# Optimization experiments

Hardware: AMD Instinct MI355X
Metric: run time of the kernel (lower is better)

The kernel has to match this reference:

```python
import jax, jax.numpy as jnp
import numpy as np

VOCAB, EMB, HID = 256, 32, 128
B, T = 512, 512


def setup_inputs() -> dict:
    key = jax.random.key(0)
    ks = jax.random.split(key, 8)
    s_emb = 1.0  # torch nn.Embedding default N(0,1)
    s_lstm = 1.0 / np.sqrt(HID)  # torch LSTM uniform(-1/sqrt(H), 1/sqrt(H))
    s_cls = 1.0 / np.sqrt(HID)
    return {
        "inputs": jax.random.randint(ks[0], (B, T), 0, VOCAB, dtype=jnp.int64),
        "emb": jax.random.normal(ks[1], (VOCAB, EMB), jnp.float32) * s_emb,
        "W_ih": jax.random.uniform(ks[2], (4 * HID, EMB), jnp.float32, -s_lstm, s_lstm),
        "W_hh": jax.random.uniform(ks[3], (4 * HID, HID), jnp.float32, -s_lstm, s_lstm),
        "b_ih": jax.random.uniform(ks[4], (4 * HID,), jnp.float32, -s_lstm, s_lstm),
        "b_hh": jax.random.uniform(ks[5], (4 * HID,), jnp.float32, -s_lstm, s_lstm),
        "W_cls": jax.random.uniform(ks[6], (VOCAB, HID), jnp.float32, -s_cls, s_cls),
        "b_cls": jax.random.uniform(ks[7], (VOCAB,), jnp.float32, -s_cls, s_cls),
    }


def reference(inputs, emb, W_ih, W_hh, b_ih, b_hh, W_cls, b_cls):
    x = emb[inputs]  # [B, T, E]
    H = W_hh.shape[1]
    # Precompute input projections for all timesteps (batched GEMM): [B, T, 4H]
    xw = jnp.einsum("bte,ge->btg", x, W_ih) + b_ih + b_hh
    xw_t = jnp.transpose(xw, (1, 0, 2))  # [T, B, 4H]

    def step(carry, xw_step):
        h, c = carry
        gates = xw_step + h @ W_hh.T  # [B, 4H]
        i, f, g, o = jnp.split(gates, 4, axis=-1)  # torch gate order: i, f, g, o
        i = jax.nn.sigmoid(i)
        f = jax.nn.sigmoid(f)
        g = jnp.tanh(g)
        o = jax.nn.sigmoid(o)
        c = f * c + i * g
        h = o * jnp.tanh(c)
        return (h, c), None

    h0 = jnp.zeros((x.shape[0], H), x.dtype)
    c0 = jnp.zeros((x.shape[0], H), x.dtype)
    (h_last, _), _ = jax.lax.scan(step, (h0, c0), xw_t)
    # classifier on last hidden state: [B, vocab]
    return h_last @ W_cls.T + b_cls
```

## Files before the change

### kernel.cpp

```cpp
#include <hip/hip_runtime.h>
#include <hip/hip_bf16.h>

#define VOCAB 256
#define EMB   32
#define HID   128
#define GATES 512
#define BATCH 512
#define SEQ   512

typedef __attribute__((ext_vector_type(8))) short bf16x8;
typedef __attribute__((ext_vector_type(4))) float f32x4;

static __device__ __forceinline__ unsigned short f2bf(float f) {
  unsigned int u = __float_as_uint(f);
  return (unsigned short)((u + 0x7fffu + ((u >> 16) & 1u)) >> 16);
}

__global__ __launch_bounds__(256) void prep_kernel(
    const float* __restrict__ emb, const float* __restrict__ W_ih,
    const float* __restrict__ W_hh, const float* __restrict__ b_ih,
    const float* __restrict__ b_hh, float* __restrict__ P,
    unsigned short* __restrict__ Whh_bf) {
  const int wg  = blockIdx.x;
  const int tid = threadIdx.x;
  if (wg < VOCAB) {
    __shared__ float e[EMB];
    if (tid < EMB) e[tid] = emb[wg * EMB + tid];
    __syncthreads();
    for (int g = tid; g < GATES; g += 256) {
      float acc = b_ih[g] + b_hh[g];
      const float* w = W_ih + g * EMB;
      #pragma unroll
      for (int k = 0; k < EMB; ++k) acc += e[k] * w[k];
      P[wg * GATES + g] = acc;
    }
  } else {
    const int base = (wg - VOCAB) * 1024 + tid * 4;
    const float4 v = *(const float4*)(W_hh + base);
    ushort4 o;
    o.x = f2bf(v.x); o.y = f2bf(v.y); o.z = f2bf(v.z); o.w = f2bf(v.w);
    *(ushort4*)(Whh_bf + base) = o;
  }
}

#define HSTRIDE 144

__global__ __launch_bounds__(512, 2) void lstm_kernel(
    const int* __restrict__ inputs, const float* __restrict__ P,
    const unsigned short* __restrict__ Whh_bf,
    const float* __restrict__ W_cls, const float* __restrict__ b_cls,
    float* __restrict__ out) {
  const int wg   = blockIdx.x;
  const int tid  = threadIdx.x;
  const int wave = tid >> 6;
  const int lane = tid & 63;
  const int c16  = lane & 15;
  const int kg   = lane >> 4;
  const int b0   = wg * 4;

  const int row   = kg;
  const int jfull = wave * 16 + c16;

  __shared__ unsigned char  chars[4][SEQ];
  __shared__ unsigned short hbuf[2][4][HSTRIDE];
  __shared__ float          h_last[4][HID];

  for (int k = tid; k < 4 * SEQ; k += 512) {
    const int r = k >> 9, t = k & (SEQ - 1);
    chars[r][t] = (unsigned char)(inputs[(b0 + r) * SEQ + t] & 0xff);
  }
  for (int k = tid; k < 2 * 4 * HSTRIDE; k += 512) ((unsigned short*)hbuf)[k] = 0;

  bf16x8 Bfrag[4][4];
  #pragma unroll
  for (int gt = 0; gt < 4; ++gt) {
    const int g = gt * 128 + wave * 16 + c16;
    #pragma unroll
    for (int ks = 0; ks < 4; ++ks)
      Bfrag[gt][ks] = *(const bf16x8*)(Whh_bf + g * HID + ks * 32 + kg * 8);
  }

  const int aoff = (c16 & 3) * HSTRIDE + kg * 8;
  const float* Pj = P + jfull;
  float cstate = 0.f;
  float hv = 0.f;

  __syncthreads();

  const float* Pr0 = Pj + (size_t)chars[row][0] * GATES;
  float p0 = Pr0[0], p1 = Pr0[128], p2 = Pr0[256], p3 = Pr0[384];

  #pragma unroll 1
  for (int t = 0; t < SEQ; ++t) {
    const int rb = t & 1;

    const int chn = chars[row][(t + 1) & (SEQ - 1)];
    const float* Pn = Pj + (size_t)chn * GATES;
    const float q0 = Pn[0], q1 = Pn[128], q2 = Pn[256], q3 = Pn[384];

    const unsigned short* hb = &hbuf[rb][0][0] + aoff;
    f32x4 acc[4] = {};
    __builtin_amdgcn_s_setprio(1);
    #pragma unroll
    for (int ks = 0; ks < 4; ++ks) {
      const bf16x8 A = *(const bf16x8*)(hb + ks * 32);
      #pragma unroll
      for (int gt = 0; gt < 4; ++gt)
        acc[gt] = __builtin_amdgcn_mfma_f32_16x16x32_bf16(A, Bfrag[gt][ks], acc[gt], 0, 0, 0);
    }
    __builtin_amdgcn_s_setprio(0);

    const float gi = (kg & 2) ? ((kg & 1) ? acc[0][3] : acc[0][2])
                              : ((kg & 1) ? acc[0][1] : acc[0][0]);
    const float gf = (kg & 2) ? ((kg & 1) ? acc[1][3] : acc[1][2])
                              : ((kg & 1) ? acc[1][1] : acc[1][0]);
    const float gg = (kg & 2) ? ((kg & 1) ? acc[2][3] : acc[2][2])
                              : ((kg & 1) ? acc[2][1] : acc[2][0]);
    const float go = (kg & 2) ? ((kg & 1) ? acc[3][3] : acc[3][2])
                              : ((kg & 1) ? acc[3][1] : acc[3][0]);

    const float ip = gi + p0;
    const float fp = gf + p1;
    const float gp = gg + p2;
    const float op = go + p3;
    const float iv = __builtin_amdgcn_rcpf(1.f + __expf(-ip));
    const float fv = __builtin_amdgcn_rcpf(1.f + __expf(-fp));
    const float gv = 1.f - 2.f * __builtin_amdgcn_rcpf(__expf(2.f * gp) + 1.f);
    const float ov = __builtin_amdgcn_rcpf(1.f + __expf(-op));
    cstate = fv * cstate + iv * gv;
    const float th = 1.f - 2.f * __builtin_amdgcn_rcpf(__expf(2.f * cstate) + 1.f);
    hv = ov * th;

    hbuf[rb ^ 1][row][jfull] = f2bf(hv);

    p0 = q0; p1 = q1; p2 = q2; p3 = q3;
    __syncthreads();
  }

  h_last[row][jfull] = hv;
  __syncthreads();

  const int erow = tid >> 7;
  const int ej   = tid & 127;
  #pragma unroll
  for (int half = 0; half < 2; ++half) {
    const int v = ej + half * 128;
    float acc = b_cls[v];
    const float4* w  = (const float4*)(W_cls + v * HID);
    const float4* hh = (const float4*)&h_last[erow][0];
    #pragma unroll
    for (int k = 0; k < HID / 4; ++k) {
      const float4 wv = w[k];
      const float4 hv4 = hh[k];
      acc += wv.x * hv4.x + wv.y * hv4.y + wv.z * hv4.z + wv.w * hv4.w;
    }
    out[(b0 + erow) * VOCAB + v] = acc;
  }
}

extern "C" void kernel_launch(void* const* d_in, const int* in_sizes, int n_in,
                              void* d_out, int out_size, void* d_ws, size_t ws_size,
                              hipStream_t stream) {
  const int*   inputs = (const int*)d_in[0];
  const float* emb    = (const float*)d_in[1];
  const float* W_ih   = (const float*)d_in[2];
  const float* W_hh   = (const float*)d_in[3];
  const float* b_ih   = (const float*)d_in[4];
  const float* b_hh   = (const float*)d_in[5];
  const float* W_cls  = (const float*)d_in[6];
  const float* b_cls  = (const float*)d_in[7];
  float* outp = (float*)d_out;

  float* Ptab = (float*)d_ws;
  unsigned short* Whh_bf = (unsigned short*)((char*)d_ws + VOCAB * GATES * sizeof(float));

  prep_kernel<<<VOCAB + 64, 256, 0, stream>>>(emb, W_ih, W_hh, b_ih, b_hh, Ptab, Whh_bf);
  lstm_kernel<<<BATCH / 4, 512, 0, stream>>>(inputs, Ptab, Whh_bf, W_cls, b_cls, outp);
}
```

Baseline: 355.1 us.

## Prescale gate weights for exp2, seed MFMA accumulators with input projection

Result: slower. 369.1 us (+4.0%).

```diff
diff --git a/kernel.cpp b/kernel.cpp
--- a/kernel.cpp
+++ b/kernel.cpp
@@ -7,6 +7,18 @@
 #define GATES 512
 #define BATCH 512
 #define SEQ   512
+#define HSTRIDE 144
+
+#define LOG2E 1.442695041f
+#if __has_builtin(__builtin_amdgcn_exp2f)
+#define GEXP(x) __builtin_amdgcn_exp2f(x)
+#define SCALE_IFO LOG2E
+#define SCALE_G   (2.0f * LOG2E)
+#else
+#define GEXP(x) __expf(x)
+#define SCALE_IFO 1.0f
+#define SCALE_G   2.0f
+#endif
 
 typedef __attribute__((ext_vector_type(8))) short bf16x8;
 typedef __attribute__((ext_vector_type(4))) float f32x4;
@@ -32,18 +44,19 @@
       const float* w = W_ih + g * EMB;
       #pragma unroll
       for (int k = 0; k < EMB; ++k) acc += e[k] * w[k];
-      P[wg * GATES + g] = acc;
+      const float sc = ((g >> 7) == 2) ? SCALE_G : SCALE_IFO;
+      P[wg * GATES + g] = acc * sc;
     }
   } else {
     const int base = (wg - VOCAB) * 1024 + tid * 4;
+    const float sc = (((base >> 14) & 3) == 2) ? SCALE_G : SCALE_IFO;
     const float4 v = *(const float4*)(W_hh + base);
     ushort4 o;
-    o.x = f2bf(v.x); o.y = f2bf(v.y); o.z = f2bf(v.z); o.w = f2bf(v.w);
+    o.x = f2bf(v.x * sc); o.y = f2bf(v.y * sc);
+    o.z = f2bf(v.z * sc); o.w = f2bf(v.w * sc);
     *(ushort4*)(Whh_bf + base) = o;
   }
 }
-
-#define HSTRIDE 144
 
 __global__ __launch_bounds__(512, 2) void lstm_kernel(
     const int* __restrict__ inputs, const float* __restrict__ P,
@@ -61,15 +74,16 @@
   const int row   = kg;
   const int jfull = wave * 16 + c16;
 
-  __shared__ unsigned char  chars[4][SEQ];
-  __shared__ unsigned short hbuf[2][4][HSTRIDE];
+  __shared__ unsigned int   offs[SEQ][4];
+  __shared__ unsigned short hbufA[4 * HSTRIDE];
+  __shared__ unsigned short hbufB[4 * HSTRIDE];
   __shared__ float          h_last[4][HID];
 
   for (int k = tid; k < 4 * SEQ; k += 512) {
-    const int r = k >> 9, t = k & (SEQ - 1);
-    chars[r][t] = (unsigned char)(inputs[(b0 + r) * SEQ + t] & 0xff);
-  }
-  for (int k = tid; k < 2 * 4 * HSTRIDE; k += 512) ((unsigned short*)hbuf)[k] = 0;
+    const int r = k & 3, t = k >> 2;
+    offs[t][r] = ((unsigned int)(inputs[(b0 + r) * SEQ + t] & 0xff)) << 9;
+  }
+  for (int k = tid; k < 4 * HSTRIDE; k += 512) { hbufA[k] = 0; hbufB[k] = 0; }
 
   bf16x8 Bfrag[4][4];
   #pragma unroll
@@ -81,61 +95,89 @@
   }
 
   const int aoff = (c16 & 3) * HSTRIDE + kg * 8;
-  const float* Pj = P + jfull;
   float cstate = 0.f;
   float hv = 0.f;
 
   __syncthreads();
 
-  const float* Pr0 = Pj + (size_t)chars[row][0] * GATES;
-  float p0 = Pr0[0], p1 = Pr0[128], p2 = Pr0[256], p3 = Pr0[384];
+  f32x4 pcur[4];
+  {
+    const uint4 o4 = *(const uint4*)&offs[0][0];
+    const float* r0 = P + o4.x + jfull;
+    const float* r1 = P + o4.y + jfull;
+    const float* r2 = P + o4.z + jfull;
+    const float* r3 = P + o4.w + jfull;
+    #pragma unroll
+    for (int gt = 0; gt < 4; ++gt) {
+      pcur[gt][0] = r0[gt * 128]; pcur[gt][1] = r1[gt * 128];
+      pcur[gt][2] = r2[gt * 128]; pcur[gt][3] = r3[gt * 128];
+    }
+  }
+
+#define STEP(HIN, HOUT, T)                                                     \
+  {                                                                            \
+                     \
+    const uint4 o4 = *(const uint4*)&offs[((T) + 1) & (SEQ - 1)][0];           \
+    f32x4 pn0, pn1, pn2, pn3;                                                  \
+    {                                                                          \
+      const float* r0 = P + o4.x + jfull;                                      \
+      const float* r1 = P + o4.y + jfull;                                      \
+      const float* r2 = P + o4.z + jfull;                                      \
+      const float* r3 = P + o4.w + jfull;                                      \
+      pn0[0] = r0[0];   pn0[1] = r1[0];   pn0[2] = r2[0];   pn0[3] = r3[0];    \
+      pn1[0] = r0[128]; pn1[1] = r1[128]; pn1[2] = r2[128]; pn1[3] = r3[128];  \
+      pn2[0] = r0[256]; pn2[1] = r1[256]; pn2[2] = r2[256]; pn2[3] = r3[256];  \
+      pn3[0] = r0[384]; pn3[1] = r1[384]; pn3[2] = r2[384]; pn3[3] = r3[384];  \
+    }                                                                          \
+    const unsigned short* hb = (HIN) + aoff;                                   \
+    const bf16x8 A0 = *(const bf16x8*)(hb);                                    \
+    const bf16x8 A1 = *(const bf16x8*)(hb + 32);                               \
+    const bf16x8 A2 = *(const bf16x8*)(hb + 64);                               \
+    const bf16x8 A3 = *(const bf16x8*)(hb + 96);                               \
+    f32x4 a0 = pcur[0], a1 = pcur[1], a2 = pcur[2], a3 = pcur[3];              \
+    a0 = __builtin_amdgcn_mfma_f32_16x16x32_bf16(A0, Bfrag[0][0], a0, 0,0,0);  \
+    a1 = __builtin_amdgcn_mfma_f32_16x16x32_bf16(A0, Bfrag[1][0], a1, 0,0,0);  \
+    a2 = __builtin_amdgcn_mfma_f32_16x16x32_bf16(A0, Bfrag[2][0], a2, 0,0,0);  \
+    a3 = __builtin_amdgcn_mfma_f32_16x16x32_bf16(A0, Bfrag[3][0], a3, 0,0,0);  \
+    a0 = __builtin_amdgcn_mfma_f32_16x16x32_bf16(A1, Bfrag[0][1], a0, 0,0,0);  \
+    a1 = __builtin_amdgcn_mfma_f32_16x16x32_bf16(A1, Bfrag[1][1], a1, 0,0,0);  \
+    a2 = __builtin_amdgcn_mfma_f32_16x16x32_bf16(A1, Bfrag[2][1], a2, 0,0,0);  \
+    a3 = __builtin_amdgcn_mfma_f32_16x16x32_bf16(A1, Bfrag[3][1], a3, 0,0,0);  \
+    a0 = __builtin_amdgcn_mfma_f32_16x16x32_bf16(A2, Bfrag[0][2], a0, 0,0,0);  \
+    a1 = __builtin_amdgcn_mfma_f32_16x16x32_bf16(A2, Bfrag[1][2], a1, 0,0,0);  \
+    a2 = __builtin_amdgcn_mfma_f32_16x16x32_bf16(A2, Bfrag[2][2], a2, 0,0,0);  \
+    a3 = __builtin_amdgcn_mfma_f32_16x16x32_bf16(A2, Bfrag[3][2], a3, 0,0,0);  \
+    a0 = __builtin_amdgcn_mfma_f32_16x16x32_bf16(A3, Bfrag[0][3], a0, 0,0,0);  \
+    a1 = __builtin_amdgcn_mfma_f32_16x16x32_bf16(A3, Bfrag[1][3], a1, 0,0,0);  \
+    a2 = __builtin_amdgcn_mfma_f32_16x16x32_bf16(A3, Bfrag[2][3], a2, 0,0,0);  \
+    a3 = __builtin_amdgcn_mfma_f32_16x16x32_bf16(A3, Bfrag[3][3], a3, 0,0,0);  \
+    const float gi = (kg & 2) ? ((kg & 1) ? a0[3] : a0[2])                     \
+                              : ((kg & 1) ? a0[1] : a0[0]);                    \
+    const float gf = (kg & 2) ? ((kg & 1) ? a1[3] : a1[2])                     \
+                              : ((kg & 1) ? a1[1] : a1[0]);                    \
+    const float gg = (kg & 2) ? ((kg & 1) ? a2[3] : a2[2])                     \
+                              : ((kg & 1) ? a2[1] : a2[0]);                    \
+    const float go = (kg & 2) ? ((kg & 1) ? a3[3] : a3[2])                     \
+                              : ((kg & 1) ? a3[1] : a3[0]);                    \
+    const float iv = __builtin_amdgcn_rcpf(1.f + GEXP(-gi));                   \
+    const float fv = __builtin_amdgcn_rcpf(1.f + GEXP(-gf));                   \
+    const float gv = 1.f - 2.f * __builtin_amdgcn_rcpf(GEXP(gg) + 1.f);        \
+    const float ov = __builtin_amdgcn_rcpf(1.f + GEXP(-go));                   \
+    cstate = fv * cstate + iv * gv;                                            \
+    const float th =                                                           \
+        1.f - 2.f * __builtin_amdgcn_rcpf(GEXP(cstate * SCALE_G) + 1.f);       \
+    hv = ov * th;                                                              \
+    (HOUT)[row * HSTRIDE + jfull] = f2bf(hv);                                  \
+    pcur[0] = pn0; pcur[1] = pn1; pcur[2] = pn2; pcur[3] = pn3;                \
+    __syncthreads();                                                           \
+  }
 
   #pragma unroll 1
-  for (int t = 0; t < SEQ; ++t) {
-    const int rb = t & 1;
-
-    const int chn = chars[row][(t + 1) & (SEQ - 1)];
-    const float* Pn = Pj + (size_t)chn * GATES;
-    const float q0 = Pn[0], q1 = Pn[128], q2 = Pn[256], q3 = Pn[384];
-
-    const unsigned short* hb = &hbuf[rb][0][0] + aoff;
-    f32x4 acc[4] = {};
-    __builtin_amdgcn_s_setprio(1);
-    #pragma unroll
-    for (int ks = 0; ks < 4; ++ks) {
-      const bf16x8 A = *(const bf16x8*)(hb + ks * 32);
-      #pragma unroll
-      for (int gt = 0; gt < 4; ++gt)
-        acc[gt] = __builtin_amdgcn_mfma_f32_16x16x32_bf16(A, Bfrag[gt][ks], acc[gt], 0, 0, 0);
-    }
-    __builtin_amdgcn_s_setprio(0);
-
-    const float gi = (kg & 2) ? ((kg & 1) ? acc[0][3] : acc[0][2])
-                              : ((kg & 1) ? acc[0][1] : acc[0][0]);
-    const float gf = (kg & 2) ? ((kg & 1) ? acc[1][3] : acc[1][2])
-                              : ((kg & 1) ? acc[1][1] : acc[1][0]);
-    const float gg = (kg & 2) ? ((kg & 1) ? acc[2][3] : acc[2][2])
-                              : ((kg & 1) ? acc[2][1] : acc[2][0]);
-    const float go = (kg & 2) ? ((kg & 1) ? acc[3][3] : acc[3][2])
-                              : ((kg & 1) ? acc[3][1] : acc[3][0]);
-
-    const float ip = gi + p0;
-    const float fp = gf + p1;
-    const float gp = gg + p2;
-    const float op = go + p3;
-    const float iv = __builtin_amdgcn_rcpf(1.f + __expf(-ip));
-    const float fv = __builtin_amdgcn_rcpf(1.f + __expf(-fp));
-    const float gv = 1.f - 2.f * __builtin_amdgcn_rcpf(__expf(2.f * gp) + 1.f);
-    const float ov = __builtin_amdgcn_rcpf(1.f + __expf(-op));
-    cstate = fv * cstate + iv * gv;
-    const float th = 1.f - 2.f * __builtin_amdgcn_rcpf(__expf(2.f * cstate) + 1.f);
-    hv = ov * th;
-
-    hbuf[rb ^ 1][row][jfull] = f2bf(hv);
-
-    p0 = q0; p1 = q1; p2 = q2; p3 = q3;
-    __syncthreads();
-  }
+  for (int t = 0; t < SEQ; t += 2) {
+    STEP(hbufA, hbufB, t)
+    STEP(hbufB, hbufA, t + 1)
+  }
+#undef STEP
 
   h_last[row][jfull] = hv;
   __syncthreads();
```
